# Kernel optimization log

Measured on AMD Instinct MI355X. Metric: run time of the kernel, lower is better.

## Reference

```python
import jax, jax.numpy as jnp
import numpy as np

UNITS = 2048

def _cat_complex(Wr, Wi):
    # real-matrix representation of complex matmul: [[Wr, -Wi], [Wi, Wr]]
    top = jnp.concatenate([Wr, -Wi], axis=-1)
    bot = jnp.concatenate([Wi, Wr], axis=-1)
    return jnp.concatenate([top, bot], axis=0)

def _hard_sigmoid(x):
    return jnp.clip(0.2 * x + 0.5, 0.0, 1.0)

def setup_inputs() -> dict:
    key = jax.random.key(0)
    ks = jax.random.split(key, 8)
    B, IN2, U3 = 1024, 4096, 3 * UNITS
    s_in = 1.0 / np.sqrt(IN2)
    s_h = 1.0 / np.sqrt(2 * UNITS)
    return {
        "inputs": jax.random.normal(ks[0], (B, IN2), jnp.float32),
        "h_tm1": jax.random.normal(ks[1], (B, 2 * UNITS), jnp.float32),
        "real_kernel": jax.random.normal(ks[2], (IN2 // 2, U3), jnp.float32) * s_in,
        "imaginary_kernel": jax.random.normal(ks[3], (IN2 // 2, U3), jnp.float32) * s_in,
        "real_recurrent_kernel": jax.random.normal(ks[4], (UNITS, U3), jnp.float32) * s_h,
        "imaginary_recurrent_kernel": jax.random.normal(ks[5], (UNITS, U3), jnp.float32) * s_h,
        "real_bias": jax.random.normal(ks[6], (U3,), jnp.float32) * 0.01,
        "imaginary_bias": jax.random.normal(ks[7], (U3,), jnp.float32) * 0.01,
    }

def reference(inputs, h_tm1, real_kernel, imaginary_kernel,
              real_recurrent_kernel, imaginary_recurrent_kernel,
              real_bias, imaginary_bias):
    u = UNITS
    # per-gate complex kernels in real [[Wr,-Wi],[Wi,Wr]] form
    Kz = _cat_complex(real_kernel[:, :u], imaginary_kernel[:, :u])
    Kr = _cat_complex(real_kernel[:, u:2 * u], imaginary_kernel[:, u:2 * u])
    Kh = _cat_complex(real_kernel[:, 2 * u:], imaginary_kernel[:, 2 * u:])
    Rz = _cat_complex(real_recurrent_kernel[:, :u], imaginary_recurrent_kernel[:, :u])
    Rr = _cat_complex(real_recurrent_kernel[:, u:2 * u], imaginary_recurrent_kernel[:, u:2 * u])
    Rh = _cat_complex(real_recurrent_kernel[:, 2 * u:], imaginary_recurrent_kernel[:, 2 * u:])
    bz = jnp.concatenate([real_bias[:u], imaginary_bias[:u]])
    br = jnp.concatenate([real_bias[u:2 * u], imaginary_bias[u:2 * u]])
    bh = jnp.concatenate([real_bias[2 * u:], imaginary_bias[2 * u:]])
    # implementation=1, reset_after=False, no dropout
    x_z = inputs @ Kz + bz
    x_r = inputs @ Kr + br
    x_h = inputs @ Kh + bh
    z = _hard_sigmoid(x_z + h_tm1 @ Rz)
    r = _hard_sigmoid(x_r + h_tm1 @ Rr)
    hh = jnp.tanh(x_h + (r * h_tm1) @ Rh)
    h = z * h_tm1 + (1.0 - z) * hh
    return h
```

## Files before the change

kernel.cpp:

```cpp
#include <hip/hip_runtime.h>

typedef _Float16 half8  __attribute__((ext_vector_type(8)));
typedef _Float16 half4v __attribute__((ext_vector_type(4)));
typedef _Float16 half2v __attribute__((ext_vector_type(2)));
typedef float    float4v __attribute__((ext_vector_type(4)));

__device__ __forceinline__ float hsig(float x) {
  return fminf(fmaxf(fmaf(x, 0.2f, 0.5f), 0.0f), 1.0f);
}

__global__ __launch_bounds__(256) void cvt_pair(const float* __restrict__ src,
                                                _Float16* __restrict__ d1,
                                                _Float16* __restrict__ d2) {
  int i = blockIdx.x * blockDim.x + threadIdx.x;
  int base = i * 4;
  int j = base & 4095;
  float s = (j < 2048) ? -1.0f : 1.0f;
  float4 v = *(const float4*)&src[base];
  half4v h1 = {(_Float16)v.x, (_Float16)v.y, (_Float16)v.z, (_Float16)v.w};
  half4v h2 = {(_Float16)(s * v.x), (_Float16)(s * v.y), (_Float16)(s * v.z), (_Float16)(s * v.w)};
  *(half4v*)&d1[base] = h1;
  *(half4v*)&d2[base] = h2;
}

__global__ __launch_bounds__(256) void transpose_cast(
    const float* __restrict__ s0, const float* __restrict__ s1,
    const float* __restrict__ s2, const float* __restrict__ s3,
    _Float16* __restrict__ d0, _Float16* __restrict__ d1m,
    _Float16* __restrict__ d2m, _Float16* __restrict__ d3m)
{
  __shared__ float tile[64][65];
  const float* srcs[4] = {s0, s1, s2, s3};
  _Float16*    dsts[4] = {d0, d1m, d2m, d3m};
  const float* src = srcs[blockIdx.z];
  _Float16*    dst = dsts[blockIdx.z];

  const int tid = threadIdx.x;
  const int k0 = blockIdx.x * 64;
  const int j0 = blockIdx.y * 64;

  const int tx = tid & 63, ty = tid >> 6;
#pragma unroll
  for (int r = 0; r < 64; r += 4)
    tile[r + ty][tx] = src[(size_t)(k0 + r + ty) * 6144 + j0 + tx];
  __syncthreads();

  const int txk = (tid & 31) * 2;
  const int tyn = tid >> 5;
#pragma unroll
  for (int r = 0; r < 64; r += 8) {
    int jl = r + tyn;
    half2v p = {(_Float16)tile[txk][jl], (_Float16)tile[txk + 1][jl]};
    *(half2v*)&dst[(size_t)(j0 + jl) * 2048 + k0 + txk] = p;
  }
}

__global__ __launch_bounds__(256) void rgate(const _Float16* __restrict__ xacc,
                                             const float* __restrict__ h,
                                             _Float16* __restrict__ A1r,
                                             _Float16* __restrict__ A2r) {
  int i = blockIdx.x * blockDim.x + threadIdx.x;
  int base = i * 4;
  int m = base >> 12;
  int j = base & 4095;
  float s = (j < 2048) ? -1.0f : 1.0f;
  half4v rp = *(const half4v*)&xacc[(size_t)m * 12288 + 4096 + j];
  float4 hv = *(const float4*)&h[base];
  float p0 = hsig((float)rp[0]) * hv.x;
  float p1 = hsig((float)rp[1]) * hv.y;
  float p2 = hsig((float)rp[2]) * hv.z;
  float p3 = hsig((float)rp[3]) * hv.w;
  half4v o1 = {(_Float16)p0, (_Float16)p1, (_Float16)p2, (_Float16)p3};
  half4v o2 = {(_Float16)(s * p0), (_Float16)(s * p1), (_Float16)(s * p2), (_Float16)(s * p3)};
  *(half4v*)&A1r[base] = o1;
  *(half4v*)&A2r[base] = o2;
}

__global__ __launch_bounds__(256) void combine(const _Float16* __restrict__ xacc,
                                               const _Float16* __restrict__ P0,
                                               const _Float16* __restrict__ P1,
                                               const float* __restrict__ h,
                                               float* __restrict__ out) {
  int i = blockIdx.x * blockDim.x + threadIdx.x;
  int base = i * 4;
  int m = base >> 12;
  int j = base & 4095;
  half4v zv = *(const half4v*)&xacc[(size_t)m * 12288 + j];
  half4v xh = *(const half4v*)&xacc[(size_t)m * 12288 + 8192 + j];
  half4v p0 = *(const half4v*)&P0[base];
  half4v p1 = *(const half4v*)&P1[base];
  float4 hv = *(const float4*)&h[base];
  float4 o;
  {
    float z = hsig((float)zv[0]); float t = tanhf((float)xh[0] + (float)p0[0] + (float)p1[0]);
    o.x = z * hv.x + (1.0f - z) * t;
  }
  {
    float z = hsig((float)zv[1]); float t = tanhf((float)xh[1] + (float)p0[1] + (float)p1[1]);
    o.y = z * hv.y + (1.0f - z) * t;
  }
  {
    float z = hsig((float)zv[2]); float t = tanhf((float)xh[2] + (float)p0[2] + (float)p1[2]);
    o.z = z * hv.z + (1.0f - z) * t;
  }
  {
    float z = hsig((float)zv[3]); float t = tanhf((float)xh[3] + (float)p0[3] + (float)p1[3]);
    o.w = z * hv.w + (1.0f - z) * t;
  }
  *(float4*)&out[base] = o;
}

template<int FINAL>
__global__ __launch_bounds__(256, 3) void gemm_big(
    const _Float16* __restrict__ Ax1, const _Float16* __restrict__ Ax2,
    const _Float16* __restrict__ Ah1, const _Float16* __restrict__ Ah2,
    const _Float16* __restrict__ WKr, const _Float16* __restrict__ WKi,
    const _Float16* __restrict__ WRr, const _Float16* __restrict__ WRi,
    _Float16* __restrict__ xacc,
    _Float16* __restrict__ P0, _Float16* __restrict__ P1,
    const float* __restrict__ rbias, const float* __restrict__ ibias)
{
  __shared__ __align__(16) _Float16 lds[16384];
  const int tid  = threadIdx.x;
  const int lane = tid & 63;
  const int wave = tid >> 6;
  const int quad = lane >> 4;
  const int r16  = lane & 15;
  const int wm = (wave >> 1) * 64;
  const int wn = (wave & 1) * 64;
  const int mbase = blockIdx.y * 128;
  const int nbase = blockIdx.x * 128;

  const int  gate   = nbase >> 12;
  const bool hi     = (nbase & 2048) != 0;
  const int  jprime = nbase & 2047;

  int nph;
  const _Float16* pA[4];
  const _Float16* pB[4];
  if (FINAL) {
    nph = 1;
    const _Float16* Ax = hi ? Ax2 : Ax1;
    const _Float16* BL = hi ? WKi : WKr;
    const _Float16* BH = hi ? WKr : WKi;
    if (blockIdx.z == 0) {
      pA[0] = Ax + (size_t)mbase * 4096;
      pB[0] = BL + (size_t)jprime * 2048;
    } else {
      pA[0] = Ax + (size_t)mbase * 4096 + 2048;
      pB[0] = BH + (size_t)jprime * 2048;
    }
  } else {
    const size_t browK = (size_t)(gate * 2048 + jprime) * 2048;
    const _Float16* Ax = hi ? Ax2 : Ax1;
    const _Float16* KL = hi ? WKi : WKr;
    const _Float16* KH = hi ? WKr : WKi;
    pA[0] = Ax + (size_t)mbase * 4096;      pB[0] = KL + browK;
    pA[1] = pA[0] + 2048;                   pB[1] = KH + browK;
    if (gate < 2) {
      nph = 4;
      const _Float16* Ah = hi ? Ah2 : Ah1;
      const _Float16* RL = hi ? WRi : WRr;
      const _Float16* RH = hi ? WRr : WRi;
      pA[2] = Ah + (size_t)mbase * 4096;    pB[2] = RL + browK;
      pA[3] = pA[2] + 2048;                 pB[3] = RH + browK;
    } else {
      nph = 2;
    }
  }

  float4v acc[4][4];
#pragma unroll
  for (int i = 0; i < 4; ++i)
#pragma unroll
    for (int j = 0; j < 4; ++j) acc[i][j] = (float4v){0.f, 0.f, 0.f, 0.f};

  int offA[4], offB[4], ldsA[4], ldsB[4];
#pragma unroll
  for (int i = 0; i < 4; ++i) {
    int c = i * 256 + tid;
    int row = c >> 3;
    int sw = (c & 7) ^ (row & 7);
    offA[i] = row * 4096 + sw * 8;
    offB[i] = row * 2048 + sw * 8;
    ldsA[i] = c * 8;
    ldsB[i] = 8192 + c * 8;
  }

#pragma unroll 1
  for (int p = 0; p < 4; ++p) {
    if (p >= nph) break;
    const _Float16* Ab = pA[p];
    const _Float16* Bb = pB[p];
#pragma unroll 1
    for (int it = 0; it < 32; ++it) {
#pragma unroll
      for (int i = 0; i < 4; ++i)
        __builtin_amdgcn_global_load_lds(
            (__attribute__((address_space(1))) void*)(Ab + offA[i]),
            (__attribute__((address_space(3))) void*)&lds[ldsA[i]], 16, 0, 0);
#pragma unroll
      for (int i = 0; i < 4; ++i)
        __builtin_amdgcn_global_load_lds(
            (__attribute__((address_space(1))) void*)(Bb + offB[i]),
            (__attribute__((address_space(3))) void*)&lds[ldsB[i]], 16, 0, 0);
      Ab += 64;
      Bb += 64;
      __syncthreads();
#pragma unroll
      for (int ks = 0; ks < 2; ++ks) {
        half8 af[4], bf[4];
        int akg = ks * 4 + quad;
#pragma unroll
        for (int t = 0; t < 4; ++t) {
          int arow = wm + t * 16 + r16;
          af[t] = *(const half8*)&lds[(arow * 8 + (akg ^ (arow & 7))) * 8];
          int brow = wn + t * 16 + r16;
          bf[t] = *(const half8*)&lds[8192 + (brow * 8 + (akg ^ (brow & 7))) * 8];
        }
#pragma unroll
        for (int mt = 0; mt < 4; ++mt)
#pragma unroll
          for (int nt = 0; nt < 4; ++nt)
            acc[mt][nt] = __builtin_amdgcn_mfma_f32_16x16x32_f16(af[mt], bf[nt], acc[mt][nt], 0, 0, 0);
      }
      __syncthreads();
    }
  }

  const int mrow0 = mbase + wm + quad * 4;
  const int ncol0 = nbase + wn + r16;
  if (!FINAL) {
#pragma unroll
    for (int nt = 0; nt < 4; ++nt) {
      int n = ncol0 + nt * 16;
      int g = n >> 12, j = n & 4095;
      float b = (j < 2048) ? rbias[g * 2048 + j] : ibias[g * 2048 + j - 2048];
#pragma unroll
      for (int mt = 0; mt < 4; ++mt)
#pragma unroll
        for (int e = 0; e < 4; ++e) {
          int m = mrow0 + mt * 16 + e;
          xacc[(size_t)m * 12288 + n] = (_Float16)(acc[mt][nt][e] + b);
        }
    }
  } else {
    _Float16* P = blockIdx.z ? P1 : P0;
#pragma unroll
    for (int nt = 0; nt < 4; ++nt) {
      int n = ncol0 + nt * 16;
#pragma unroll
      for (int mt = 0; mt < 4; ++mt)
#pragma unroll
        for (int e = 0; e < 4; ++e) {
          int m = mrow0 + mt * 16 + e;
          P[(size_t)m * 4096 + n] = (_Float16)acc[mt][nt][e];
        }
    }
  }
}

extern "C" void kernel_launch(void* const* d_in, const int* in_sizes, int n_in,
                              void* d_out, int out_size, void* d_ws, size_t ws_size,
                              hipStream_t stream) {
  const float* inputs = (const float*)d_in[0];
  const float* h_tm1  = (const float*)d_in[1];
  const float* rk     = (const float*)d_in[2];
  const float* ik     = (const float*)d_in[3];
  const float* rrk    = (const float*)d_in[4];
  const float* irk    = (const float*)d_in[5];
  const float* rb     = (const float*)d_in[6];
  const float* ib     = (const float*)d_in[7];
  float* out = (float*)d_out;

  char* ws = (char*)d_ws;
  _Float16* WrK  = (_Float16*)(ws + 0);
  _Float16* WiK  = (_Float16*)(ws + 25165824);
  _Float16* WrR  = (_Float16*)(ws + 50331648);
  _Float16* WiR  = (_Float16*)(ws + 75497472);
  _Float16* A1x  = (_Float16*)(ws + 100663296);
  _Float16* A2x  = (_Float16*)(ws + 109051904);
  _Float16* A1h  = (_Float16*)(ws + 117440512);
  _Float16* A2h  = (_Float16*)(ws + 125829120);
  _Float16* xacc = (_Float16*)(ws + 134217728);
  _Float16* A1r  = A1x;
  _Float16* A2r  = A2x;
  _Float16* P0   = A1h;
  _Float16* P1   = A2h;

  cvt_pair<<<4096, 256, 0, stream>>>(inputs, A1x, A2x);
  cvt_pair<<<4096, 256, 0, stream>>>(h_tm1, A1h, A2h);
  transpose_cast<<<dim3(32, 96, 4), 256, 0, stream>>>(rk, ik, rrk, irk, WrK, WiK, WrR, WiR);
  gemm_big<0><<<dim3(96, 8), 256, 0, stream>>>(A1x, A2x, A1h, A2h, WrK, WiK, WrR, WiR,
                                               xacc, nullptr, nullptr, rb, ib);
  rgate<<<4096, 256, 0, stream>>>(xacc, h_tm1, A1r, A2r);
  gemm_big<1><<<dim3(32, 8, 2), 256, 0, stream>>>(A1r, A2r, nullptr, nullptr,
                                                  WrR + (size_t)4096 * 2048,
                                                  WiR + (size_t)4096 * 2048,
                                                  nullptr, nullptr, nullptr, P0, P1,
                                                  nullptr, nullptr);
  combine<<<4096, 256, 0, stream>>>(xacc, P0, P1, h_tm1, out);
}
```

Before: 512.9 us.

## Split GEMM work into uniform-length blocks and widen transpose and conversion loads

The first GEMM used blocks of unequal length, since z/r gates also ran the recurrent product. It now runs 160 blocks of uniform K length. Recurrent partials for z/r go to a separate buffer, and a fused r-gate kernel adds them back together with the bias. The final recurrent GEMM is split-K into four partial outputs, which combine sums. The two input conversions merge into one launch, the weight transpose uses float4 loads and half8 stores, and launch bounds rise to 5 waves per SIMD. This is meant to fix load imbalance and low block counts, at the cost of extra partial-sum traffic and fp16 rounding of the partials.

```diff
diff --git a/kernel.cpp b/kernel.cpp
--- a/kernel.cpp
+++ b/kernel.cpp
@@ -2,17 +2,20 @@
 
 typedef _Float16 half8  __attribute__((ext_vector_type(8)));
 typedef _Float16 half4v __attribute__((ext_vector_type(4)));
-typedef _Float16 half2v __attribute__((ext_vector_type(2)));
 typedef float    float4v __attribute__((ext_vector_type(4)));
 
 __device__ __forceinline__ float hsig(float x) {
   return fminf(fmaxf(fmaf(x, 0.2f, 0.5f), 0.0f), 1.0f);
 }
 
-__global__ __launch_bounds__(256) void cvt_pair(const float* __restrict__ src,
-                                                _Float16* __restrict__ d1,
-                                                _Float16* __restrict__ d2) {
-  int i = blockIdx.x * blockDim.x + threadIdx.x;
+__global__ __launch_bounds__(256) void cvt_pair(const float* __restrict__ x,
+                                                const float* __restrict__ h,
+                                                _Float16* __restrict__ d1x, _Float16* __restrict__ d2x,
+                                                _Float16* __restrict__ d1h, _Float16* __restrict__ d2h) {
+  const float* src = blockIdx.y ? h : x;
+  _Float16* d1 = blockIdx.y ? d1h : d1x;
+  _Float16* d2 = blockIdx.y ? d2h : d2x;
+  int i = blockIdx.x * 256 + threadIdx.x;
   int base = i * 4;
   int j = base & 4095;
   float s = (j < 2048) ? -1.0f : 1.0f;
@@ -39,85 +42,39 @@
   const int k0 = blockIdx.x * 64;
   const int j0 = blockIdx.y * 64;
 
-  const int tx = tid & 63, ty = tid >> 6;
-#pragma unroll
-  for (int r = 0; r < 64; r += 4)
-    tile[r + ty][tx] = src[(size_t)(k0 + r + ty) * 6144 + j0 + tx];
+  const int rr = tid >> 4;
+  const int c4 = (tid & 15) * 4;
+#pragma unroll
+  for (int it = 0; it < 4; ++it) {
+    int row = it * 16 + rr;
+    float4 v = *(const float4*)&src[(size_t)(k0 + row) * 6144 + j0 + c4];
+    tile[row][c4]     = v.x;
+    tile[row][c4 + 1] = v.y;
+    tile[row][c4 + 2] = v.z;
+    tile[row][c4 + 3] = v.w;
+  }
   __syncthreads();
-
-  const int txk = (tid & 31) * 2;
-  const int tyn = tid >> 5;
-#pragma unroll
-  for (int r = 0; r < 64; r += 8) {
-    int jl = r + tyn;
-    half2v p = {(_Float16)tile[txk][jl], (_Float16)tile[txk + 1][jl]};
-    *(half2v*)&dst[(size_t)(j0 + jl) * 2048 + k0 + txk] = p;
-  }
-}
-
-__global__ __launch_bounds__(256) void rgate(const _Float16* __restrict__ xacc,
-                                             const float* __restrict__ h,
-                                             _Float16* __restrict__ A1r,
-                                             _Float16* __restrict__ A2r) {
-  int i = blockIdx.x * blockDim.x + threadIdx.x;
-  int base = i * 4;
-  int m = base >> 12;
-  int j = base & 4095;
-  float s = (j < 2048) ? -1.0f : 1.0f;
-  half4v rp = *(const half4v*)&xacc[(size_t)m * 12288 + 4096 + j];
-  float4 hv = *(const float4*)&h[base];
-  float p0 = hsig((float)rp[0]) * hv.x;
-  float p1 = hsig((float)rp[1]) * hv.y;
-  float p2 = hsig((float)rp[2]) * hv.z;
-  float p3 = hsig((float)rp[3]) * hv.w;
-  half4v o1 = {(_Float16)p0, (_Float16)p1, (_Float16)p2, (_Float16)p3};
-  half4v o2 = {(_Float16)(s * p0), (_Float16)(s * p1), (_Float16)(s * p2), (_Float16)(s * p3)};
-  *(half4v*)&A1r[base] = o1;
-  *(half4v*)&A2r[base] = o2;
-}
-
-__global__ __launch_bounds__(256) void combine(const _Float16* __restrict__ xacc,
-                                               const _Float16* __restrict__ P0,
-                                               const _Float16* __restrict__ P1,
-                                               const float* __restrict__ h,
-                                               float* __restrict__ out) {
-  int i = blockIdx.x * blockDim.x + threadIdx.x;
-  int base = i * 4;
-  int m = base >> 12;
-  int j = base & 4095;
-  half4v zv = *(const half4v*)&xacc[(size_t)m * 12288 + j];
-  half4v xh = *(const half4v*)&xacc[(size_t)m * 12288 + 8192 + j];
-  half4v p0 = *(const half4v*)&P0[base];
-  half4v p1 = *(const half4v*)&P1[base];
-  float4 hv = *(const float4*)&h[base];
-  float4 o;
-  {
-    float z = hsig((float)zv[0]); float t = tanhf((float)xh[0] + (float)p0[0] + (float)p1[0]);
-    o.x = z * hv.x + (1.0f - z) * t;
-  }
-  {
-    float z = hsig((float)zv[1]); float t = tanhf((float)xh[1] + (float)p0[1] + (float)p1[1]);
-    o.y = z * hv.y + (1.0f - z) * t;
-  }
-  {
-    float z = hsig((float)zv[2]); float t = tanhf((float)xh[2] + (float)p0[2] + (float)p1[2]);
-    o.z = z * hv.z + (1.0f - z) * t;
-  }
-  {
-    float z = hsig((float)zv[3]); float t = tanhf((float)xh[3] + (float)p0[3] + (float)p1[3]);
-    o.w = z * hv.w + (1.0f - z) * t;
-  }
-  *(float4*)&out[base] = o;
-}
-
-template<int FINAL>
-__global__ __launch_bounds__(256, 3) void gemm_big(
+  const int k8 = (tid & 7) * 8;
+  const int jb = tid >> 3;
+#pragma unroll
+  for (int it = 0; it < 2; ++it) {
+    int jl = it * 32 + jb;
+    half8 hv;
+#pragma unroll
+    for (int i = 0; i < 8; ++i) hv[i] = (_Float16)tile[k8 + i][jl];
+    *(half8*)&dst[(size_t)(j0 + jl) * 2048 + k0 + k8] = hv;
+  }
+}
+
+template<int MODE>
+__global__ __launch_bounds__(256, 5) void gemm_big(
     const _Float16* __restrict__ Ax1, const _Float16* __restrict__ Ax2,
     const _Float16* __restrict__ Ah1, const _Float16* __restrict__ Ah2,
     const _Float16* __restrict__ WKr, const _Float16* __restrict__ WKi,
     const _Float16* __restrict__ WRr, const _Float16* __restrict__ WRi,
-    _Float16* __restrict__ xacc,
+    _Float16* __restrict__ xacc, _Float16* __restrict__ PH,
     _Float16* __restrict__ P0, _Float16* __restrict__ P1,
+    _Float16* __restrict__ P2, _Float16* __restrict__ P3,
     const float* __restrict__ rbias, const float* __restrict__ ibias)
 {
   __shared__ __align__(16) _Float16 lds[16384];
@@ -129,44 +86,50 @@
   const int wm = (wave >> 1) * 64;
   const int wn = (wave & 1) * 64;
   const int mbase = blockIdx.y * 128;
-  const int nbase = blockIdx.x * 128;
-
-  const int  gate   = nbase >> 12;
-  const bool hi     = (nbase & 2048) != 0;
-  const int  jprime = nbase & 2047;
-
-  int nph;
-  const _Float16* pA[4];
-  const _Float16* pB[4];
-  if (FINAL) {
-    nph = 1;
-    const _Float16* Ax = hi ? Ax2 : Ax1;
+
+  constexpr int nit = MODE ? 16 : 32;
+  constexpr int nph = MODE ? 1 : 2;
+
+  const _Float16* pA[2];
+  const _Float16* pB[2];
+  _Float16* dst;
+  int ldc;
+  int n0;
+  bool wb;
+
+  if (MODE == 0) {
+    const int bx = blockIdx.x;
+    bool useH;
+    if (bx < 128) { n0 = (bx >> 1) * 128; useH = (bx & 1); }
+    else          { n0 = 8192 + (bx - 128) * 128; useH = false; }
+    const int  gate = n0 >> 12;
+    const bool hi   = (n0 & 2048) != 0;
+    const int  jp   = n0 & 2047;
+    const size_t brow = (size_t)(gate * 2048 + jp) * 2048;
+    const _Float16* Aa = useH ? (hi ? Ah2 : Ah1) : (hi ? Ax2 : Ax1);
+    const _Float16* BL = useH ? (hi ? WRi : WRr) : (hi ? WKi : WKr);
+    const _Float16* BH = useH ? (hi ? WRr : WRi) : (hi ? WKr : WKi);
+    pA[0] = Aa + (size_t)mbase * 4096;  pB[0] = BL + brow;
+    pA[1] = pA[0] + 2048;               pB[1] = BH + brow;
+    if (useH) { dst = PH;   ldc = 8192;  }
+    else      { dst = xacc; ldc = 12288; }
+    wb = (bx >= 128);
+  } else {
+    n0 = blockIdx.x * 128;
+    const bool hi = (n0 & 2048) != 0;
+    const int  jp = n0 & 2047;
+    const int z  = blockIdx.z;
+    const int zz = z >> 1;
+    const int koff = (z & 1) * 1024;
+    const _Float16* Aa = hi ? Ax2 : Ax1;
     const _Float16* BL = hi ? WKi : WKr;
     const _Float16* BH = hi ? WKr : WKi;
-    if (blockIdx.z == 0) {
-      pA[0] = Ax + (size_t)mbase * 4096;
-      pB[0] = BL + (size_t)jprime * 2048;
-    } else {
-      pA[0] = Ax + (size_t)mbase * 4096 + 2048;
-      pB[0] = BH + (size_t)jprime * 2048;
-    }
-  } else {
-    const size_t browK = (size_t)(gate * 2048 + jprime) * 2048;
-    const _Float16* Ax = hi ? Ax2 : Ax1;
-    const _Float16* KL = hi ? WKi : WKr;
-    const _Float16* KH = hi ? WKr : WKi;
-    pA[0] = Ax + (size_t)mbase * 4096;      pB[0] = KL + browK;
-    pA[1] = pA[0] + 2048;                   pB[1] = KH + browK;
-    if (gate < 2) {
-      nph = 4;
-      const _Float16* Ah = hi ? Ah2 : Ah1;
-      const _Float16* RL = hi ? WRi : WRr;
-      const _Float16* RH = hi ? WRr : WRi;
-      pA[2] = Ah + (size_t)mbase * 4096;    pB[2] = RL + browK;
-      pA[3] = pA[2] + 2048;                 pB[3] = RH + browK;
-    } else {
-      nph = 2;
-    }
+    pA[0] = Aa + (size_t)mbase * 4096 + zz * 2048 + koff;
+    pB[0] = (zz ? BH : BL) + (size_t)jp * 2048 + koff;
+    pA[1] = pA[0]; pB[1] = pB[0];
+    dst = (z == 0) ? P0 : (z == 1) ? P1 : (z == 2) ? P2 : P3;
+    ldc = 4096;
+    wb = false;
   }
 
   float4v acc[4][4];
@@ -188,12 +151,11 @@
   }
 
 #pragma unroll 1
-  for (int p = 0; p < 4; ++p) {
-    if (p >= nph) break;
+  for (int p = 0; p < nph; ++p) {
     const _Float16* Ab = pA[p];
     const _Float16* Bb = pB[p];
 #pragma unroll 1
-    for (int it = 0; it < 32; ++it) {
+    for (int it = 0; it < nit; ++it) {
 #pragma unroll
       for (int i = 0; i < 4; ++i)
         __builtin_amdgcn_global_load_lds(
@@ -229,35 +191,91 @@
   }
 
   const int mrow0 = mbase + wm + quad * 4;
-  const int ncol0 = nbase + wn + r16;
-  if (!FINAL) {
-#pragma unroll
-    for (int nt = 0; nt < 4; ++nt) {
-      int n = ncol0 + nt * 16;
+  const int ncol0 = wn + r16;
+#pragma unroll
+  for (int nt = 0; nt < 4; ++nt) {
+    int nl = ncol0 + nt * 16;
+    float b = 0.0f;
+    if (wb) {
+      int n = n0 + nl;
       int g = n >> 12, j = n & 4095;
-      float b = (j < 2048) ? rbias[g * 2048 + j] : ibias[g * 2048 + j - 2048];
-#pragma unroll
-      for (int mt = 0; mt < 4; ++mt)
-#pragma unroll
-        for (int e = 0; e < 4; ++e) {
-          int m = mrow0 + mt * 16 + e;
-          xacc[(size_t)m * 12288 + n] = (_Float16)(acc[mt][nt][e] + b);
-        }
+      b = (j < 2048) ? rbias[g * 2048 + j] : ibias[g * 2048 + j - 2048];
     }
-  } else {
-    _Float16* P = blockIdx.z ? P1 : P0;
-#pragma unroll
-    for (int nt = 0; nt < 4; ++nt) {
-      int n = ncol0 + nt * 16;
-#pragma unroll
-      for (int mt = 0; mt < 4; ++mt)
-#pragma unroll
-        for (int e = 0; e < 4; ++e) {
-          int m = mrow0 + mt * 16 + e;
-          P[(size_t)m * 4096 + n] = (_Float16)acc[mt][nt][e];
-        }
-    }
-  }
+#pragma unroll
+    for (int mt = 0; mt < 4; ++mt)
+#pragma unroll
+      for (int e = 0; e < 4; ++e) {
+        int m = mrow0 + mt * 16 + e;
+        dst[(size_t)m * ldc + n0 + nl] = (_Float16)(acc[mt][nt][e] + b);
+      }
+  }
+}
+
+__global__ __launch_bounds__(256) void rgate_fuse(
+    _Float16* __restrict__ xacc,
+    const _Float16* __restrict__ PH,
+    const float* __restrict__ h,
+    const float* __restrict__ rb, const float* __restrict__ ib,
+    _Float16* __restrict__ A1r, _Float16* __restrict__ A2r)
+{
+  int i = blockIdx.x * 256 + threadIdx.x;
+  int m = i >> 10;
+  int j = (i & 1023) * 4;
+  float s = (j < 2048) ? -1.0f : 1.0f;
+
+  half4v xz = *(const half4v*)&xacc[(size_t)m * 12288 + j];
+  half4v hz = *(const half4v*)&PH[(size_t)m * 8192 + j];
+  float4 bz = *(const float4*)((j < 2048) ? &rb[j] : &ib[j - 2048]);
+  half4v zo;
+  zo[0] = (_Float16)((float)xz[0] + (float)hz[0] + bz.x);
+  zo[1] = (_Float16)((float)xz[1] + (float)hz[1] + bz.y);
+  zo[2] = (_Float16)((float)xz[2] + (float)hz[2] + bz.z);
+  zo[3] = (_Float16)((float)xz[3] + (float)hz[3] + bz.w);
+  *(half4v*)&xacc[(size_t)m * 12288 + j] = zo;
+
+  half4v xr = *(const half4v*)&xacc[(size_t)m * 12288 + 4096 + j];
+  half4v hr = *(const half4v*)&PH[(size_t)m * 8192 + 4096 + j];
+  float4 br = *(const float4*)((j < 2048) ? &rb[2048 + j] : &ib[2048 + j - 2048]);
+  float4 hv = *(const float4*)&h[(size_t)m * 4096 + j];
+  float p0 = hsig((float)xr[0] + (float)hr[0] + br.x) * hv.x;
+  float p1 = hsig((float)xr[1] + (float)hr[1] + br.y) * hv.y;
+  float p2 = hsig((float)xr[2] + (float)hr[2] + br.z) * hv.z;
+  float p3 = hsig((float)xr[3] + (float)hr[3] + br.w) * hv.w;
+  half4v o1 = {(_Float16)p0, (_Float16)p1, (_Float16)p2, (_Float16)p3};
+  half4v o2 = {(_Float16)(s * p0), (_Float16)(s * p1), (_Float16)(s * p2), (_Float16)(s * p3)};
+  size_t o = (size_t)m * 4096 + j;
+  *(half4v*)&A1r[o] = o1;
+  *(half4v*)&A2r[o] = o2;
+}
+
+__global__ __launch_bounds__(256) void combine(const _Float16* __restrict__ xacc,
+                                               const _Float16* __restrict__ P0,
+                                               const _Float16* __restrict__ P1,
+                                               const _Float16* __restrict__ P2,
+                                               const _Float16* __restrict__ P3,
+                                               const float* __restrict__ h,
+                                               float* __restrict__ out) {
+  int i = blockIdx.x * 256 + threadIdx.x;
+  int base = i * 4;
+  int m = base >> 12;
+  int j = base & 4095;
+  half4v zv = *(const half4v*)&xacc[(size_t)m * 12288 + j];
+  half4v xh = *(const half4v*)&xacc[(size_t)m * 12288 + 8192 + j];
+  half4v p0 = *(const half4v*)&P0[base];
+  half4v p1 = *(const half4v*)&P1[base];
+  half4v p2 = *(const half4v*)&P2[base];
+  half4v p3 = *(const half4v*)&P3[base];
+  float4 hv = *(const float4*)&h[base];
+  float4 o;
+#pragma unroll
+  for (int e = 0; e < 4; ++e) {
+    float z = hsig((float)zv[e]);
+    float t = tanhf((float)xh[e] + (float)p0[e] + (float)p1[e] + (float)p2[e] + (float)p3[e]);
+    float hval = (e == 0) ? hv.x : (e == 1) ? hv.y : (e == 2) ? hv.z : hv.w;
+    float r = z * hval + (1.0f - z) * t;
+    if (e == 0) o.x = r; else if (e == 1) o.y = r; else if (e == 2) o.z = r; else o.w = r;
+  }
+  *(float4*)&out[base] = o;
 }
 
 extern "C" void kernel_launch(void* const* d_in, const int* in_sizes, int n_in,
@@ -283,21 +301,24 @@
   _Float16* A1h  = (_Float16*)(ws + 117440512);
   _Float16* A2h  = (_Float16*)(ws + 125829120);
   _Float16* xacc = (_Float16*)(ws + 134217728);
-  _Float16* A1r  = A1x;
-  _Float16* A2r  = A2x;
-  _Float16* P0   = A1h;
-  _Float16* P1   = A2h;
-
-  cvt_pair<<<4096, 256, 0, stream>>>(inputs, A1x, A2x);
-  cvt_pair<<<4096, 256, 0, stream>>>(h_tm1, A1h, A2h);
+  _Float16* PH   = (_Float16*)(ws + 159383552);
+  _Float16* A1r = A1x;
+  _Float16* A2r = A2x;
+  _Float16* P0  = A1h;
+  _Float16* P1  = A2h;
+  _Float16* P2  = (_Float16*)(ws + 0);
+  _Float16* P3  = (_Float16*)(ws + 8388608);
+
+  cvt_pair<<<dim3(4096, 2), 256, 0, stream>>>(inputs, h_tm1, A1x, A2x, A1h, A2h);
   transpose_cast<<<dim3(32, 96, 4), 256, 0, stream>>>(rk, ik, rrk, irk, WrK, WiK, WrR, WiR);
-  gemm_big<0><<<dim3(96, 8), 256, 0, stream>>>(A1x, A2x, A1h, A2h, WrK, WiK, WrR, WiR,
-                                               xacc, nullptr, nullptr, rb, ib);
-  rgate<<<4096, 256, 0, stream>>>(xacc, h_tm1, A1r, A2r);
-  gemm_big<1><<<dim3(32, 8, 2), 256, 0, stream>>>(A1r, A2r, nullptr, nullptr,
+  gemm_big<0><<<dim3(160, 8), 256, 0, stream>>>(A1x, A2x, A1h, A2h, WrK, WiK, WrR, WiR,
+                                                xacc, PH, nullptr, nullptr, nullptr, nullptr,
+                                                rb, ib);
+  rgate_fuse<<<4096, 256, 0, stream>>>(xacc, PH, h_tm1, rb, ib, A1r, A2r);
+  gemm_big<1><<<dim3(32, 8, 4), 256, 0, stream>>>(A1r, A2r, nullptr, nullptr,
                                                   WrR + (size_t)4096 * 2048,
                                                   WiR + (size_t)4096 * 2048,
-                                                  nullptr, nullptr, nullptr, P0, P1,
-                                                  nullptr, nullptr);
-  combine<<<4096, 256, 0, stream>>>(xacc, P0, P1, h_tm1, out);
-}
+                                                  nullptr, nullptr, nullptr, nullptr,
+                                                  P0, P1, P2, P3, nullptr, nullptr);
+  combine<<<4096, 256, 0, stream>>>(xacc, P0, P1, P2, P3, h_tm1, out);
+}
```

Measured after the change: 792.5 us. 1.55x slower.
